# Performance work log

Measured on AMD Instinct MI355X. Metric: run time of the kernel, lower is better.

The kernel has to match this reference:

```python
import jax, jax.numpy as jnp
import numpy as np

B, C_IN, H, W = 8, 64, 256, 256
C_OUT, K, N_KERNELS = 128, 3, 8
PAD = K // 2


def setup_inputs() -> dict:
    key = jax.random.key(0)
    k1, k2, k3, k4 = jax.random.split(key, 4)
    x = jax.random.normal(k1, (B, C_IN, H, W), dtype=jnp.float32)
    kernel_bank = jax.random.normal(k2, (N_KERNELS, C_OUT, C_IN, K, K), dtype=jnp.float32)
    # nn.Linear(in_channels, num_kernels): weight (N, C_IN), bias (N,)
    lim = 1.0 / np.sqrt(C_IN)
    attn_w = jax.random.uniform(k3, (N_KERNELS, C_IN), minval=-lim, maxval=lim, dtype=jnp.float32)
    attn_b = jax.random.uniform(k4, (N_KERNELS,), minval=-lim, maxval=lim, dtype=jnp.float32)
    return {"x": x, "kernel_bank": kernel_bank, "attn_w": attn_w, "attn_b": attn_b}


def _per_sample_conv(xi, wi):
    # xi: (C_IN, H, W), wi: (C_OUT, C_IN, K, K)
    out = jax.lax.conv_general_dilated(
        xi[None], wi, window_strides=(1, 1), padding=[(PAD, PAD), (PAD, PAD)],
        dimension_numbers=("NCHW", "OIHW", "NCHW"))
    return out[0]


def reference(x, kernel_bank, attn_w, attn_b):
    pooled = jnp.mean(x, axis=(2, 3))                      # (B, C_IN)
    logits = pooled @ attn_w.T + attn_b                     # (B, N)
    attn = jax.nn.softmax(logits, axis=1)                   # (B, N)
    # Fused kernel mix: avoid (B, N, O, I, K, K) intermediate
    mixed = jnp.einsum("bn,noihw->boihw", attn, kernel_bank)  # (B, O, I, K, K)
    return jax.vmap(_per_sample_conv)(x, mixed)             # (B, O, H, W)
```

## Files before the change

### kernel.cpp

```cpp
#include <hip/hip_runtime.h>
#include <hip/hip_bf16.h>

#define B_     8
#define C_IN   64
#define C_OUT  128
#define HW     256
#define NK     8
#define KS     3

typedef __attribute__((ext_vector_type(8))) short bf16x8;
typedef __attribute__((ext_vector_type(4))) float f32x4;
typedef __attribute__((ext_vector_type(4))) unsigned int u32x4;

__device__ inline unsigned short f2bf(float f) {
    union { float f; unsigned int u; } a; a.f = f;
    unsigned int u = a.u;
    u += 0x7fffu + ((u >> 16) & 1u);
    return (unsigned short)(u >> 16);
}
__device__ inline float bf2f(unsigned short u) {
    union { float f; unsigned int u; } a; a.u = ((unsigned int)u) << 16; return a.f;
}

#define XT_PLANE  (258 * 64)
#define SLAB_B    16640

__global__ __launch_bounds__(256) void prepass_kernel(const float* __restrict__ x,
                                                      unsigned short* __restrict__ xT,
                                                      float* __restrict__ pooled) {
    const int hp = blockIdx.x;
    const int b  = blockIdx.y;
    const int t  = threadIdx.x;
    unsigned short* plane = xT + ((size_t)b * 258 + hp) * XT_PLANE;

    if (hp == 0 || hp == 257) {
        f32x4 z = {0.f, 0.f, 0.f, 0.f};
        for (int ofs = t * 16; ofs < XT_PLANE * 2; ofs += 256 * 16)
            *(f32x4*)((char*)plane + ofs) = z;
        return;
    }
    const int h = hp - 1;

    __shared__ unsigned short tile[256 * 66];
    __shared__ float psum[4][64];

    const float* xp = x + ((size_t)b * C_IN * HW + h) * HW + t;
    unsigned int pk[32];
    #pragma unroll
    for (int ci = 0; ci < 32; ci++) {
        float v0 = xp[(size_t)(2 * ci) * (HW * HW)];
        float v1 = xp[(size_t)(2 * ci + 1) * (HW * HW)];
        unsigned int p = (unsigned int)f2bf(v0) | ((unsigned int)f2bf(v1) << 16);
        pk[ci] = p;
        *(unsigned int*)&tile[t * 66 + 2 * ci] = p;
    }

    unsigned short* rowp = plane + (size_t)(t + 1) * 64;
    const int sw = (t + 1) & 7;
    #pragma unroll
    for (int j = 0; j < 8; j++) {
        u32x4 v; v[0] = pk[4*j]; v[1] = pk[4*j+1]; v[2] = pk[4*j+2]; v[3] = pk[4*j+3];
        *(u32x4*)(rowp + (size_t)((j ^ sw) * 8)) = v;
    }
    if (t < 2) {
        unsigned short* zr = plane + (size_t)(t ? 257 : 0) * 64;
        f32x4 z = {0.f, 0.f, 0.f, 0.f};
        #pragma unroll
        for (int j = 0; j < 8; j++) *(f32x4*)((char*)zr + j * 16) = z;
    }

    __syncthreads();
    const int c = t & 63, part = t >> 6;
    float s = 0.f;
    #pragma unroll 8
    for (int i = 0; i < 64; i++)
        s += bf2f(tile[(part * 64 + i) * 66 + c]);
    psum[part][c] = s;
    __syncthreads();
    if (t < 64) {
        float tot = (psum[0][t] + psum[1][t]) + (psum[2][t] + psum[3][t]);
        atomicAdd(pooled + b * C_IN + t, tot * (1.0f / (HW * HW)));
    }
}

__global__ void attn_kernel(const float* __restrict__ pooled,
                            const float* __restrict__ attn_w,
                            const float* __restrict__ attn_b,
                            float* __restrict__ attn) {
    const int t = threadIdx.x;
    const int b = t >> 3, n = t & 7;
    float s = attn_b[n];
    #pragma unroll 8
    for (int c = 0; c < C_IN; c++) s += pooled[b * C_IN + c] * attn_w[n * C_IN + c];
    __shared__ float logits[B_ * NK];
    logits[t] = s;
    __syncthreads();
    float m = -1e30f;
    #pragma unroll
    for (int j = 0; j < NK; j++) m = fmaxf(m, logits[b * NK + j]);
    float denom = 0.f;
    #pragma unroll
    for (int j = 0; j < NK; j++) denom += expf(logits[b * NK + j] - m);
    attn[t] = expf(s - m) / denom;
}

__global__ __launch_bounds__(256) void mix_kernel(const float* __restrict__ bank,
                                                  const float* __restrict__ attn,
                                                  unsigned short* __restrict__ Wt2) {
    const int PER_B = C_OUT * C_IN * KS * KS;
    int idx = blockIdx.x * 256 + threadIdx.x;
    int b = idx / PER_B;
    int r = idx % PER_B;
    float s = 0.f;
    #pragma unroll
    for (int n = 0; n < NK; n++) s += attn[b * NK + n] * bank[(size_t)n * PER_B + r];
    int kw = r % 3;
    int t1 = r / 3;
    int kh = t1 % 3;
    int t2 = t1 / 3;
    int i = t2 & 63;
    int o = t2 >> 6;
    size_t off = (((size_t)((b * 3 + kh) * 3 + kw) * 2 + (i >> 5)) * 128 + o) * 32 + (i & 31);
    Wt2[off] = f2bf(s);
}

__global__ __launch_bounds__(256, 2) void conv_mfma2(const unsigned short* __restrict__ xT,
                                                     const short* __restrict__ Wt2,
                                                     float* __restrict__ out) {
    const int w0 = blockIdx.x * 128;
    const int h0 = blockIdx.y * 8;
    const int b  = blockIdx.z;
    const int t    = threadIdx.x;
    const int lane = t & 63;
    const int wid  = t >> 6;
    const int wm   = (wid & 1) * 64;
    const int wn   = (wid >> 1) * 64;
    const int l15  = lane & 15;
    const int quad = lane >> 4;

    __shared__ short sxs[4 * 8320];

    #define STAGE(HP) do {                                                            \
        const char* _src = (const char*)(xT + (((size_t)b * 258 + (size_t)(HP)) * 258 \
                                               + (size_t)w0) * 64);                   \
        char* _dst = (char*)sxs + (((HP) & 3) * SLAB_B);                              \
        const int _wo = wid * 4096;                                                   \
        __builtin_amdgcn_global_load_lds((const __attribute__((address_space(1))) void*)(_src + _wo +    lane * 16), (__attribute__((address_space(3))) void*)(_dst + _wo),        16, 0, 0); \
        __builtin_amdgcn_global_load_lds((const __attribute__((address_space(1))) void*)(_src + _wo + 1024 + lane * 16), (__attribute__((address_space(3))) void*)(_dst + _wo + 1024), 16, 0, 0); \
        __builtin_amdgcn_global_load_lds((const __attribute__((address_space(1))) void*)(_src + _wo + 2048 + lane * 16), (__attribute__((address_space(3))) void*)(_dst + _wo + 2048), 16, 0, 0); \
        __builtin_amdgcn_global_load_lds((const __attribute__((address_space(1))) void*)(_src + _wo + 3072 + lane * 16), (__attribute__((address_space(3))) void*)(_dst + _wo + 3072), 16, 0, 0); \
        __builtin_amdgcn_global_load_lds((const __attribute__((address_space(1))) void*)(_src + 16384 + lane * 4),       (__attribute__((address_space(3))) void*)(_dst + 16384),        4, 0, 0); \
    } while (0)

    const short* wt_b = Wt2 + (size_t)b * (9 * 2 * 4096);

    STAGE(h0); STAGE(h0 + 1); STAGE(h0 + 2);

    #pragma unroll 1
    for (int h = h0; h < h0 + 8; ++h) {
        __builtin_amdgcn_s_barrier();
        if (h <= h0 + 6) {
            STAGE(h + 3);
            asm volatile("s_waitcnt vmcnt(5)" ::: "memory");
        } else {
            asm volatile("s_waitcnt vmcnt(0)" ::: "memory");
        }
        __builtin_amdgcn_s_barrier();

        f32x4 acc[4][4];
        #pragma unroll
        for (int mt = 0; mt < 4; mt++)
            #pragma unroll
            for (int nt = 0; nt < 4; nt++)
                acc[mt][nt] = (f32x4){0.f, 0.f, 0.f, 0.f};

        #pragma unroll
        for (int kh = 0; kh < 3; kh++) {
            const short* buf = sxs + ((h + kh) & 3) * 8320;
            const short* wbase = wt_b + kh * (3 * 2 * 4096);
            #pragma unroll
            for (int kw = 0; kw < 3; kw++) {
                const int row = wn + l15 + kw;
                const int rx  = row & 7;
                #pragma unroll
                for (int ic = 0; ic < 2; ic++) {
                    const short* Ap = wbase + (kw * 2 + ic) * 4096 + (wm + l15) * 32 + quad * 8;
                    bf16x8 a0 = *(const bf16x8*)(Ap);
                    bf16x8 a1 = *(const bf16x8*)(Ap + 512);
                    bf16x8 a2 = *(const bf16x8*)(Ap + 1024);
                    bf16x8 a3 = *(const bf16x8*)(Ap + 1536);
                    const short* Bp = buf + row * 64 + (((ic << 2) + quad) ^ rx) * 8;
                    bf16x8 b0 = *(const bf16x8*)(Bp);
                    bf16x8 b1 = *(const bf16x8*)(Bp + 1024);
                    bf16x8 b2 = *(const bf16x8*)(Bp + 2048);
                    bf16x8 b3 = *(const bf16x8*)(Bp + 3072);
                    acc[0][0] = __builtin_amdgcn_mfma_f32_16x16x32_bf16(a0, b0, acc[0][0], 0, 0, 0);
                    acc[0][1] = __builtin_amdgcn_mfma_f32_16x16x32_bf16(a0, b1, acc[0][1], 0, 0, 0);
                    acc[0][2] = __builtin_amdgcn_mfma_f32_16x16x32_bf16(a0, b2, acc[0][2], 0, 0, 0);
                    acc[0][3] = __builtin_amdgcn_mfma_f32_16x16x32_bf16(a0, b3, acc[0][3], 0, 0, 0);
                    acc[1][0] = __builtin_amdgcn_mfma_f32_16x16x32_bf16(a1, b0, acc[1][0], 0, 0, 0);
                    acc[1][1] = __builtin_amdgcn_mfma_f32_16x16x32_bf16(a1, b1, acc[1][1], 0, 0, 0);
                    acc[1][2] = __builtin_amdgcn_mfma_f32_16x16x32_bf16(a1, b2, acc[1][2], 0, 0, 0);
                    acc[1][3] = __builtin_amdgcn_mfma_f32_16x16x32_bf16(a1, b3, acc[1][3], 0, 0, 0);
                    acc[2][0] = __builtin_amdgcn_mfma_f32_16x16x32_bf16(a2, b0, acc[2][0], 0, 0, 0);
                    acc[2][1] = __builtin_amdgcn_mfma_f32_16x16x32_bf16(a2, b1, acc[2][1], 0, 0, 0);
                    acc[2][2] = __builtin_amdgcn_mfma_f32_16x16x32_bf16(a2, b2, acc[2][2], 0, 0, 0);
                    acc[2][3] = __builtin_amdgcn_mfma_f32_16x16x32_bf16(a2, b3, acc[2][3], 0, 0, 0);
                    acc[3][0] = __builtin_amdgcn_mfma_f32_16x16x32_bf16(a3, b0, acc[3][0], 0, 0, 0);
                    acc[3][1] = __builtin_amdgcn_mfma_f32_16x16x32_bf16(a3, b1, acc[3][1], 0, 0, 0);
                    acc[3][2] = __builtin_amdgcn_mfma_f32_16x16x32_bf16(a3, b2, acc[3][2], 0, 0, 0);
                    acc[3][3] = __builtin_amdgcn_mfma_f32_16x16x32_bf16(a3, b3, acc[3][3], 0, 0, 0);
                }
            }
        }

        #pragma unroll
        for (int mt = 0; mt < 4; mt++) {
            const int o = wm + mt * 16 + quad * 4;
            #pragma unroll
            for (int nt = 0; nt < 4; nt++) {
                const int w = w0 + wn + nt * 16 + l15;
                float* op = out + (((size_t)(b * C_OUT + o) * HW + h) * HW + w);
                #pragma unroll
                for (int r = 0; r < 4; r++) op[(size_t)r * HW * HW] = acc[mt][nt][r];
            }
        }
    }
    #undef STAGE
}

__global__ __launch_bounds__(256) void pool_kernel(const float* __restrict__ x,
                                                   float* __restrict__ pooled) {
    const int plane = blockIdx.x;
    const float4* p = (const float4*)(x + (size_t)plane * HW * HW);
    float s = 0.f;
    for (int idx = threadIdx.x; idx < (HW * HW) / 4; idx += 256) {
        float4 v = p[idx];
        s += v.x + v.y + v.z + v.w;
    }
    #pragma unroll
    for (int off = 32; off > 0; off >>= 1) s += __shfl_down(s, off, 64);
    __shared__ float ls[4];
    const int lane = threadIdx.x & 63, wv = threadIdx.x >> 6;
    if (lane == 0) ls[wv] = s;
    __syncthreads();
    if (threadIdx.x == 0) {
        float t = ls[0] + ls[1] + ls[2] + ls[3];
        pooled[plane] = t * (1.0f / (HW * HW));
    }
}

__global__ __launch_bounds__(256) void conv_mfma(const float* __restrict__ x,
                                                 const short* __restrict__ Wt2,
                                                 float* __restrict__ out) {
    const int w0 = blockIdx.x * 128;
    const int h  = blockIdx.y;
    const int b  = blockIdx.z;
    const int t    = threadIdx.x;
    const int lane = t & 63;
    const int wid  = t >> 6;
    const int wm   = (wid & 1) * 64;
    const int wn   = (wid >> 1) * 64;
    const int l15  = lane & 15;
    const int quad = lane >> 4;
    __shared__ short sxs[130 * 72];
    f32x4 acc[4][4];
    #pragma unroll
    for (int mt = 0; mt < 4; mt++)
        #pragma unroll
        for (int nt = 0; nt < 4; nt++)
            acc[mt][nt] = (f32x4){0.f, 0.f, 0.f, 0.f};
    for (int kh = 0; kh < 3; kh++) {
        __syncthreads();
        const int hr = h + kh - 1;
        const bool rv = (hr >= 0) && (hr < HW);
        {
            const int wl = t & 127;
            const int w  = w0 + wl - 1;
            const bool wvalid = rv && (w >= 0) && (w < HW);
            #pragma unroll
            for (int it = 0; it < 16; it++) {
                const int ip = it * 2 + (t >> 7);
                float v0 = 0.f, v1 = 0.f;
                if (wvalid) {
                    const float* px = x + (((size_t)(b * C_IN + 2 * ip) * HW + hr) * HW + w);
                    v0 = px[0];
                    v1 = px[HW * HW];
                }
                ushort2 u;
                u.x = f2bf(v0);
                u.y = f2bf(v1);
                *(ushort2*)&sxs[wl * 72 + 2 * ip] = u;
            }
            if (t < 128) {
                const int i2  = t >> 1;
                const int wl2 = 128 + (t & 1);
                const int w2  = w0 + wl2 - 1;
                unsigned short uv = 0;
                if (rv && w2 < HW)
                    uv = f2bf(x[((size_t)(b * C_IN + i2) * HW + hr) * HW + w2]);
                ((unsigned short*)sxs)[wl2 * 72 + i2] = uv;
            }
        }
        __syncthreads();
        const short* wbase = Wt2 + (size_t)((b * 3 + kh) * 3) * 2 * 4096;
        #pragma unroll
        for (int kw = 0; kw < 3; kw++) {
            #pragma unroll
            for (int ic = 0; ic < 2; ic++) {
                const short* Ap = wbase + (size_t)(kw * 2 + ic) * 4096
                                + (wm + l15) * 32 + quad * 8;
                bf16x8 a0 = *(const bf16x8*)(Ap);
                bf16x8 a1 = *(const bf16x8*)(Ap + 512);
                bf16x8 a2 = *(const bf16x8*)(Ap + 1024);
                bf16x8 a3 = *(const bf16x8*)(Ap + 1536);
                const short* Bp = sxs + (wn + l15 + kw) * 72 + ic * 32 + quad * 8;
                bf16x8 b0 = *(const bf16x8*)(Bp);
                bf16x8 b1 = *(const bf16x8*)(Bp + 16 * 72);
                bf16x8 b2 = *(const bf16x8*)(Bp + 32 * 72);
                bf16x8 b3 = *(const bf16x8*)(Bp + 48 * 72);
                acc[0][0] = __builtin_amdgcn_mfma_f32_16x16x32_bf16(a0, b0, acc[0][0], 0, 0, 0);
                acc[0][1] = __builtin_amdgcn_mfma_f32_16x16x32_bf16(a0, b1, acc[0][1], 0, 0, 0);
                acc[0][2] = __builtin_amdgcn_mfma_f32_16x16x32_bf16(a0, b2, acc[0][2], 0, 0, 0);
                acc[0][3] = __builtin_amdgcn_mfma_f32_16x16x32_bf16(a0, b3, acc[0][3], 0, 0, 0);
                acc[1][0] = __builtin_amdgcn_mfma_f32_16x16x32_bf16(a1, b0, acc[1][0], 0, 0, 0);
                acc[1][1] = __builtin_amdgcn_mfma_f32_16x16x32_bf16(a1, b1, acc[1][1], 0, 0, 0);
                acc[1][2] = __builtin_amdgcn_mfma_f32_16x16x32_bf16(a1, b2, acc[1][2], 0, 0, 0);
                acc[1][3] = __builtin_amdgcn_mfma_f32_16x16x32_bf16(a1, b3, acc[1][3], 0, 0, 0);
                acc[2][0] = __builtin_amdgcn_mfma_f32_16x16x32_bf16(a2, b0, acc[2][0], 0, 0, 0);
                acc[2][1] = __builtin_amdgcn_mfma_f32_16x16x32_bf16(a2, b1, acc[2][1], 0, 0, 0);
                acc[2][2] = __builtin_amdgcn_mfma_f32_16x16x32_bf16(a2, b2, acc[2][2], 0, 0, 0);
                acc[2][3] = __builtin_amdgcn_mfma_f32_16x16x32_bf16(a2, b3, acc[2][3], 0, 0, 0);
                acc[3][0] = __builtin_amdgcn_mfma_f32_16x16x32_bf16(a3, b0, acc[3][0], 0, 0, 0);
                acc[3][1] = __builtin_amdgcn_mfma_f32_16x16x32_bf16(a3, b1, acc[3][1], 0, 0, 0);
                acc[3][2] = __builtin_amdgcn_mfma_f32_16x16x32_bf16(a3, b2, acc[3][2], 0, 0, 0);
                acc[3][3] = __builtin_amdgcn_mfma_f32_16x16x32_bf16(a3, b3, acc[3][3], 0, 0, 0);
            }
        }
    }
    #pragma unroll
    for (int mt = 0; mt < 4; mt++) {
        const int o = wm + mt * 16 + quad * 4;
        #pragma unroll
        for (int nt = 0; nt < 4; nt++) {
            const int w = w0 + wn + nt * 16 + l15;
            float* op = out + (((size_t)(b * C_OUT + o) * HW + h) * HW + w);
            #pragma unroll
            for (int r = 0; r < 4; r++) op[(size_t)r * HW * HW] = acc[mt][nt][r];
        }
    }
}

extern "C" void kernel_launch(void* const* d_in, const int* in_sizes, int n_in,
                              void* d_out, int out_size, void* d_ws, size_t ws_size,
                              hipStream_t stream) {
    const float* x      = (const float*)d_in[0];
    const float* bank   = (const float*)d_in[1];
    const float* attn_w = (const float*)d_in[2];
    const float* attn_b = (const float*)d_in[3];
    float* out = (float*)d_out;

    const size_t XT_BYTES  = (size_t)B_ * 258 * XT_PLANE * sizeof(short);
    const size_t WT2_BYTES = (size_t)B_ * C_OUT * C_IN * KS * KS * sizeof(short);
    const size_t NEED = XT_BYTES + WT2_BYTES + (size_t)(B_ * C_IN + B_ * NK) * 4 + 256;

    if (ws_size >= NEED) {
        unsigned short* xT  = (unsigned short*)d_ws;
        unsigned short* Wt2 = (unsigned short*)((char*)d_ws + XT_BYTES);
        float* pooled = (float*)((char*)d_ws + XT_BYTES + WT2_BYTES);
        float* attn   = pooled + B_ * C_IN;

        hipMemsetAsync(pooled, 0, B_ * C_IN * sizeof(float), stream);
        prepass_kernel<<<dim3(258, B_), 256, 0, stream>>>(x, xT, pooled);
        attn_kernel<<<1, 64, 0, stream>>>(pooled, attn_w, attn_b, attn);
        mix_kernel<<<(B_ * C_OUT * C_IN * KS * KS) / 256, 256, 0, stream>>>(bank, attn, Wt2);
        conv_mfma2<<<dim3(2, HW / 8, B_), 256, 0, stream>>>(xT, (const short*)Wt2, out);
    } else {
        unsigned short* Wt2 = (unsigned short*)d_ws;
        float* pooled = (float*)((char*)d_ws + 589824 * sizeof(short));
        float* attn   = pooled + B_ * C_IN;
        pool_kernel<<<B_ * C_IN, 256, 0, stream>>>(x, pooled);
        attn_kernel<<<1, 64, 0, stream>>>(pooled, attn_w, attn_b, attn);
        mix_kernel<<<(B_ * C_OUT * C_IN * KS * KS) / 256, 256, 0, stream>>>(bank, attn, Wt2);
        conv_mfma<<<dim3(2, HW, B_), 256, 0, stream>>>(x, (const short*)Wt2, out);
    }
}
```

Measured before the change: 478.3 us.

## Split conv tile across 8 waves and replace pooled atomics with partial sums

The conv kernel now runs 512 threads (8 waves) per block, each wave computing a 32x64 output sub-tile with half the accumulators. Staging loads are split across more waves, with matching waitcnt adjustments. This lowers register pressure and adds parallelism to hide latency, at the cost of more redundant B-fragment LDS reads per wave. Separately, the per-row atomicAdd pooling plus memset is replaced by per-row partial sums that a per-batch attention kernel reduces, removing atomic contention and one memset launch.

New measurement: 495.1 us. 3.5% more time.

```diff
diff --git a/kernel.cpp b/kernel.cpp
--- a/kernel.cpp
+++ b/kernel.cpp
@@ -27,7 +27,7 @@
 
 __global__ __launch_bounds__(256) void prepass_kernel(const float* __restrict__ x,
                                                       unsigned short* __restrict__ xT,
-                                                      float* __restrict__ pooled) {
+                                                      float* __restrict__ poolpart) {
     const int hp = blockIdx.x;
     const int b  = blockIdx.y;
     const int t  = threadIdx.x;
@@ -77,31 +77,48 @@
         s += bf2f(tile[(part * 64 + i) * 66 + c]);
     psum[part][c] = s;
     __syncthreads();
-    if (t < 64) {
-        float tot = (psum[0][t] + psum[1][t]) + (psum[2][t] + psum[3][t]);
-        atomicAdd(pooled + b * C_IN + t, tot * (1.0f / (HW * HW)));
-    }
-}
-
-__global__ void attn_kernel(const float* __restrict__ pooled,
-                            const float* __restrict__ attn_w,
-                            const float* __restrict__ attn_b,
-                            float* __restrict__ attn) {
+    if (t < 64)
+        poolpart[((size_t)b * 258 + hp) * 64 + t] =
+            (psum[0][t] + psum[1][t]) + (psum[2][t] + psum[3][t]);
+}
+
+__global__ __launch_bounds__(256) void attn_kernel(const float* __restrict__ poolpart,
+                                                   const float* __restrict__ attn_w,
+                                                   const float* __restrict__ attn_b,
+                                                   float* __restrict__ attn) {
+    const int b = blockIdx.x;
     const int t = threadIdx.x;
-    const int b = t >> 3, n = t & 7;
-    float s = attn_b[n];
-    #pragma unroll 8
-    for (int c = 0; c < C_IN; c++) s += pooled[b * C_IN + c] * attn_w[n * C_IN + c];
-    __shared__ float logits[B_ * NK];
-    logits[t] = s;
-    __syncthreads();
-    float m = -1e30f;
-    #pragma unroll
-    for (int j = 0; j < NK; j++) m = fmaxf(m, logits[b * NK + j]);
-    float denom = 0.f;
-    #pragma unroll
-    for (int j = 0; j < NK; j++) denom += expf(logits[b * NK + j] - m);
-    attn[t] = expf(s - m) / denom;
+    const int c = t & 63, part = t >> 6;
+    __shared__ float psum[4][64];
+    __shared__ float pooled[64];
+    __shared__ float logits[NK];
+
+    float s = 0.f;
+    const float* pp = poolpart + ((size_t)b * 258) * 64 + c;
+    for (int hp = part * 64 + 1; hp <= part * 64 + 64; hp++)
+        s += pp[(size_t)hp * 64];
+    psum[part][c] = s;
+    __syncthreads();
+    if (t < 64)
+        pooled[t] = ((psum[0][t] + psum[1][t]) + (psum[2][t] + psum[3][t]))
+                    * (1.0f / (HW * HW));
+    __syncthreads();
+    if (t < NK) {
+        float l = attn_b[t];
+        #pragma unroll 8
+        for (int cc = 0; cc < C_IN; cc++) l += pooled[cc] * attn_w[t * C_IN + cc];
+        logits[t] = l;
+    }
+    __syncthreads();
+    if (t < NK) {
+        float m = -1e30f;
+        #pragma unroll
+        for (int j = 0; j < NK; j++) m = fmaxf(m, logits[j]);
+        float denom = 0.f;
+        #pragma unroll
+        for (int j = 0; j < NK; j++) denom += expf(logits[j] - m);
+        attn[b * NK + t] = expf(logits[t] - m) / denom;
+    }
 }
 
 __global__ __launch_bounds__(256) void mix_kernel(const float* __restrict__ bank,
@@ -124,7 +141,7 @@
     Wt2[off] = f2bf(s);
 }
 
-__global__ __launch_bounds__(256, 2) void conv_mfma2(const unsigned short* __restrict__ xT,
+__global__ __launch_bounds__(512, 4) void conv_mfma3(const unsigned short* __restrict__ xT,
                                                      const short* __restrict__ Wt2,
                                                      float* __restrict__ out) {
     const int w0 = blockIdx.x * 128;
@@ -133,8 +150,8 @@
     const int t    = threadIdx.x;
     const int lane = t & 63;
     const int wid  = t >> 6;
-    const int wm   = (wid & 1) * 64;
-    const int wn   = (wid >> 1) * 64;
+    const int wm   = (wid >> 1) * 32;
+    const int wn   = (wid & 1) * 64;
     const int l15  = lane & 15;
     const int quad = lane >> 4;
 
@@ -144,12 +161,11 @@
         const char* _src = (const char*)(xT + (((size_t)b * 258 + (size_t)(HP)) * 258 \
                                                + (size_t)w0) * 64);                   \
         char* _dst = (char*)sxs + (((HP) & 3) * SLAB_B);                              \
-        const int _wo = wid * 4096;                                                   \
-        __builtin_amdgcn_global_load_lds((const __attribute__((address_space(1))) void*)(_src + _wo +    lane * 16), (__attribute__((address_space(3))) void*)(_dst + _wo),        16, 0, 0); \
+        const int _wo = wid * 2048;                                                   \
+        __builtin_amdgcn_global_load_lds((const __attribute__((address_space(1))) void*)(_src + _wo +        lane * 16), (__attribute__((address_space(3))) void*)(_dst + _wo),        16, 0, 0); \
         __builtin_amdgcn_global_load_lds((const __attribute__((address_space(1))) void*)(_src + _wo + 1024 + lane * 16), (__attribute__((address_space(3))) void*)(_dst + _wo + 1024), 16, 0, 0); \
-        __builtin_amdgcn_global_load_lds((const __attribute__((address_space(1))) void*)(_src + _wo + 2048 + lane * 16), (__attribute__((address_space(3))) void*)(_dst + _wo + 2048), 16, 0, 0); \
-        __builtin_amdgcn_global_load_lds((const __attribute__((address_space(1))) void*)(_src + _wo + 3072 + lane * 16), (__attribute__((address_space(3))) void*)(_dst + _wo + 3072), 16, 0, 0); \
-        __builtin_amdgcn_global_load_lds((const __attribute__((address_space(1))) void*)(_src + 16384 + lane * 4),       (__attribute__((address_space(3))) void*)(_dst + 16384),        4, 0, 0); \
+        if (wid == 7)                                                                 \
+            __builtin_amdgcn_global_load_lds((const __attribute__((address_space(1))) void*)(_src + 16384 + lane * 4),   (__attribute__((address_space(3))) void*)(_dst + 16384),        4, 0, 0); \
     } while (0)
 
     const short* wt_b = Wt2 + (size_t)b * (9 * 2 * 4096);
@@ -161,15 +177,16 @@
         __builtin_amdgcn_s_barrier();
         if (h <= h0 + 6) {
             STAGE(h + 3);
-            asm volatile("s_waitcnt vmcnt(5)" ::: "memory");
+            if (wid == 7) asm volatile("s_waitcnt vmcnt(3)" ::: "memory");
+            else          asm volatile("s_waitcnt vmcnt(2)" ::: "memory");
         } else {
             asm volatile("s_waitcnt vmcnt(0)" ::: "memory");
         }
         __builtin_amdgcn_s_barrier();
 
-        f32x4 acc[4][4];
-        #pragma unroll
-        for (int mt = 0; mt < 4; mt++)
+        f32x4 acc[2][4];
+        #pragma unroll
+        for (int mt = 0; mt < 2; mt++)
             #pragma unroll
             for (int nt = 0; nt < 4; nt++)
                 acc[mt][nt] = (f32x4){0.f, 0.f, 0.f, 0.f};
@@ -187,8 +204,6 @@
                     const short* Ap = wbase + (kw * 2 + ic) * 4096 + (wm + l15) * 32 + quad * 8;
                     bf16x8 a0 = *(const bf16x8*)(Ap);
                     bf16x8 a1 = *(const bf16x8*)(Ap + 512);
-                    bf16x8 a2 = *(const bf16x8*)(Ap + 1024);
-                    bf16x8 a3 = *(const bf16x8*)(Ap + 1536);
                     const short* Bp = buf + row * 64 + (((ic << 2) + quad) ^ rx) * 8;
                     bf16x8 b0 = *(const bf16x8*)(Bp);
                     bf16x8 b1 = *(const bf16x8*)(Bp + 1024);
@@ -202,20 +217,12 @@
                     acc[1][1] = __builtin_amdgcn_mfma_f32_16x16x32_bf16(a1, b1, acc[1][1], 0, 0, 0);
                     acc[1][2] = __builtin_amdgcn_mfma_f32_16x16x32_bf16(a1, b2, acc[1][2], 0, 0, 0);
                     acc[1][3] = __builtin_amdgcn_mfma_f32_16x16x32_bf16(a1, b3, acc[1][3], 0, 0, 0);
-                    acc[2][0] = __builtin_amdgcn_mfma_f32_16x16x32_bf16(a2, b0, acc[2][0], 0, 0, 0);
-                    acc[2][1] = __builtin_amdgcn_mfma_f32_16x16x32_bf16(a2, b1, acc[2][1], 0, 0, 0);
-                    acc[2][2] = __builtin_amdgcn_mfma_f32_16x16x32_bf16(a2, b2, acc[2][2], 0, 0, 0);
-                    acc[2][3] = __builtin_amdgcn_mfma_f32_16x16x32_bf16(a2, b3, acc[2][3], 0, 0, 0);
-                    acc[3][0] = __builtin_amdgcn_mfma_f32_16x16x32_bf16(a3, b0, acc[3][0], 0, 0, 0);
-                    acc[3][1] = __builtin_amdgcn_mfma_f32_16x16x32_bf16(a3, b1, acc[3][1], 0, 0, 0);
-                    acc[3][2] = __builtin_amdgcn_mfma_f32_16x16x32_bf16(a3, b2, acc[3][2], 0, 0, 0);
-                    acc[3][3] = __builtin_amdgcn_mfma_f32_16x16x32_bf16(a3, b3, acc[3][3], 0, 0, 0);
                 }
             }
         }
 
         #pragma unroll
-        for (int mt = 0; mt < 4; mt++) {
+        for (int mt = 0; mt < 2; mt++) {
             const int o = wm + mt * 16 + quad * 4;
             #pragma unroll
             for (int nt = 0; nt < 4; nt++) {
@@ -248,6 +255,27 @@
         float t = ls[0] + ls[1] + ls[2] + ls[3];
         pooled[plane] = t * (1.0f / (HW * HW));
     }
+}
+
+__global__ void attn_legacy(const float* __restrict__ pooled,
+                            const float* __restrict__ attn_w,
+                            const float* __restrict__ attn_b,
+                            float* __restrict__ attn) {
+    const int t = threadIdx.x;
+    const int b = t >> 3, n = t & 7;
+    float s = attn_b[n];
+    #pragma unroll 8
+    for (int c = 0; c < C_IN; c++) s += pooled[b * C_IN + c] * attn_w[n * C_IN + c];
+    __shared__ float logits[B_ * NK];
+    logits[t] = s;
+    __syncthreads();
+    float m = -1e30f;
+    #pragma unroll
+    for (int j = 0; j < NK; j++) m = fmaxf(m, logits[b * NK + j]);
+    float denom = 0.f;
+    #pragma unroll
+    for (int j = 0; j < NK; j++) denom += expf(logits[b * NK + j] - m);
+    attn[t] = expf(s - m) / denom;
 }
 
 __global__ __launch_bounds__(256) void conv_mfma(const float* __restrict__ x,
@@ -362,25 +390,25 @@
 
     const size_t XT_BYTES  = (size_t)B_ * 258 * XT_PLANE * sizeof(short);
     const size_t WT2_BYTES = (size_t)B_ * C_OUT * C_IN * KS * KS * sizeof(short);
-    const size_t NEED = XT_BYTES + WT2_BYTES + (size_t)(B_ * C_IN + B_ * NK) * 4 + 256;
+    const size_t PP_BYTES  = (size_t)B_ * 258 * 64 * sizeof(float);
+    const size_t NEED = XT_BYTES + WT2_BYTES + PP_BYTES + (size_t)(B_ * NK) * 4 + 256;
 
     if (ws_size >= NEED) {
         unsigned short* xT  = (unsigned short*)d_ws;
         unsigned short* Wt2 = (unsigned short*)((char*)d_ws + XT_BYTES);
-        float* pooled = (float*)((char*)d_ws + XT_BYTES + WT2_BYTES);
-        float* attn   = pooled + B_ * C_IN;
-
-        hipMemsetAsync(pooled, 0, B_ * C_IN * sizeof(float), stream);
-        prepass_kernel<<<dim3(258, B_), 256, 0, stream>>>(x, xT, pooled);
-        attn_kernel<<<1, 64, 0, stream>>>(pooled, attn_w, attn_b, attn);
+        float* poolpart = (float*)((char*)d_ws + XT_BYTES + WT2_BYTES);
+        float* attn     = poolpart + (size_t)B_ * 258 * 64;
+
+        prepass_kernel<<<dim3(258, B_), 256, 0, stream>>>(x, xT, poolpart);
+        attn_kernel<<<B_, 256, 0, stream>>>(poolpart, attn_w, attn_b, attn);
         mix_kernel<<<(B_ * C_OUT * C_IN * KS * KS) / 256, 256, 0, stream>>>(bank, attn, Wt2);
-        conv_mfma2<<<dim3(2, HW / 8, B_), 256, 0, stream>>>(xT, (const short*)Wt2, out);
+        conv_mfma3<<<dim3(2, HW / 8, B_), 512, 0, stream>>>(xT, (const short*)Wt2, out);
     } else {
         unsigned short* Wt2 = (unsigned short*)d_ws;
         float* pooled = (float*)((char*)d_ws + 589824 * sizeof(short));
         float* attn   = pooled + B_ * C_IN;
         pool_kernel<<<B_ * C_IN, 256, 0, stream>>>(x, pooled);
-        attn_kernel<<<1, 64, 0, stream>>>(pooled, attn_w, attn_b, attn);
+        attn_legacy<<<1, 64, 0, stream>>>(pooled, attn_w, attn_b, attn);
         mix_kernel<<<(B_ * C_OUT * C_IN * KS * KS) / 256, 256, 0, stream>>>(bank, attn, Wt2);
         conv_mfma<<<dim3(2, HW, B_), 256, 0, stream>>>(x, (const short*)Wt2, out);
     }
```
